# Kernel optimization log

Hardware: AMD Instinct MI355X
Metric: run time of the kernel (lower is better)

Reference implementation:

```python
import jax, jax.numpy as jnp
import numpy as np

KH = KW = 3
PAD = 1
STRIDE = 1
C_IN = 32
C_OUT = 16
H = W = 64
B = 64
H_OUT = (H - KH + 2 * PAD) // STRIDE + 1
W_OUT = (W - KW + 2 * PAD) // STRIDE + 1
S = H_OUT * W_OUT
K = C_IN * KH * KW


def unfold_2d(x):
    # x: [B, C, H, W] -> [B, C*KH*KW, S], torch.nn.functional.unfold ordering
    xp = jnp.pad(x, ((0, 0), (0, 0), (PAD, PAD), (PAD, PAD)))
    patches = []
    for i in range(KH):
        for j in range(KW):
            patches.append(xp[:, :, i:i + H_OUT * STRIDE:STRIDE, j:j + W_OUT * STRIDE:STRIDE])
    u = jnp.stack(patches, axis=2)  # [B, C, KH*KW, H_OUT, W_OUT]
    return u.reshape(x.shape[0], K, S)


def setup_inputs() -> dict:
    key = jax.random.key(0)
    k1, k2, k3 = jax.random.split(key, 3)
    X = jax.random.normal(k1, (B, C_IN, H, W), dtype=jnp.float32)
    # kaiming normal (linear): std = 1/sqrt(fan_in), fan_in = K for each location's GEMM
    weight = jax.random.normal(k2, (S, K, C_OUT), dtype=jnp.float32) / jnp.sqrt(jnp.float32(K))
    # xavier uniform over [H_OUT, W_OUT]
    lim = np.sqrt(6.0 / (H_OUT + W_OUT))
    bias = jax.random.uniform(k3, (H_OUT, W_OUT), dtype=jnp.float32, minval=-lim, maxval=lim)
    return {"X": X, "weight": weight, "bias": bias}


def reference(X, weight, bias):
    ufld = unfold_2d(X)                               # [B, K, S]
    ufld = ufld + bias.reshape(1, 1, -1)              # bias added per-location to patches
    h = jnp.einsum('bks,skc->bcs', ufld, weight)      # per-location unshared GEMM
    return h.reshape(X.shape[0], C_OUT, H_OUT, W_OUT)
```

## Files before the change

kernel.cpp:

```cpp
#include <hip/hip_runtime.h>
#include <stdint.h>
#include <stddef.h>

#define HOUT 64
#define WOUT 64
#define CIN  32
#define COUT 16
#define BATCH 64
#define SLOC 4096
#define KTOT 288
#define HPAD 66

typedef __attribute__((ext_vector_type(8))) short  short8;
typedef __attribute__((ext_vector_type(4))) float  floatx4;

static __device__ __forceinline__ unsigned short f2bf(float f) {
    union { float f; unsigned int u; } v; v.f = f;
    unsigned int u = v.u;
    unsigned int r = (u + 0x7FFFu + ((u >> 16) & 1u)) >> 16;
    return (unsigned short)r;
}

__global__ __launch_bounds__(256) void prep_kernel(const float* __restrict__ X,
                                                   unsigned short* __restrict__ xt) {
    const int id  = blockIdx.x;
    const int tid = threadIdx.x;

    if (id < 260) {
        int h1, w1;
        if (id < 66)       { h1 = 0;  w1 = id; }
        else if (id < 132) { h1 = 65; w1 = id - 66; }
        else { int r = id - 132; h1 = (r >> 1) + 1; w1 = (r & 1) ? 65 : 0; }
        ((uint4*)(xt + (size_t)(h1 * HPAD + w1) * 2048))[tid] = uint4{0u, 0u, 0u, 0u};
    }

    const int w   = tid >> 2;
    const int cg8 = (tid & 3) * 8;
#pragma unroll
    for (int u = 0; u < 2; ++u) {
        const int unit = id * 2 + u;
        const int h = unit >> 6, b = unit & 63;
        const float* xb = X + (((size_t)b * CIN + cg8) * HOUT + h) * WOUT + w;
        unsigned short v[8];
#pragma unroll
        for (int j = 0; j < 8; ++j)
            v[j] = f2bf(xb[(size_t)j * HOUT * WOUT]);
        uint4 pack;
        pack.x = (unsigned)v[0] | ((unsigned)v[1] << 16);
        pack.y = (unsigned)v[2] | ((unsigned)v[3] << 16);
        pack.z = (unsigned)v[4] | ((unsigned)v[5] << 16);
        pack.w = (unsigned)v[6] | ((unsigned)v[7] << 16);
        *(uint4*)(xt + (size_t)((h + 1) * HPAD + (w + 1)) * 2048 + b * CIN + cg8) = pack;
    }
}

__global__ __launch_bounds__(256, 4) void varconv_kernel(const unsigned short* __restrict__ xt,
                                                         const float* __restrict__ Wg,
                                                         const float* __restrict__ bias,
                                                         float* __restrict__ out) {
    __shared__ float lds[16 * 324];

    int id = blockIdx.x;
    int lo = id & 7;
    int q4 = (id >> 3) & 3;
    int g  = ((id >> 5) << 3) | lo;
    int s0 = g * 16;
    int y  = s0 >> 6;
    int x0 = s0 & 63;
    int B0 = q4 * 16;

    int lane = threadIdx.x & 63, wv = threadIdx.x >> 6;
    int q = lane >> 4;
    int n = lane & 15;

#pragma unroll
    for (int i = 0; i < 4; ++i) {
        int sl = wv * 4 + i;
        int s  = s0 + sl;
        int x  = x0 + sl;

        const unsigned short* ab = xt + (size_t)(B0 + n) * CIN + q * 8;
        short8 af[9];
#pragma unroll
        for (int t = 0; t < 9; ++t) {
            const int cy = t / 3, cx = t % 3;
            af[t] = *(const short8*)(ab + (size_t)((y + cy) * HPAD + (x + cx)) * 2048);
        }

        const float* wb = Wg + (size_t)s * (KTOT * COUT) + n;
        float csum = 0.f;
        short8 bf[9];
#pragma unroll
        for (int tg = 0; tg < 3; ++tg) {
            float wreg[3][8];
#pragma unroll
            for (int tt = 0; tt < 3; ++tt)
#pragma unroll
                for (int j = 0; j < 8; ++j)
                    wreg[tt][j] = wb[(size_t)((8 * q + j) * 9 + (tg * 3 + tt)) * COUT];
#pragma unroll
            for (int tt = 0; tt < 3; ++tt) {
                unsigned short hh[8];
#pragma unroll
                for (int j = 0; j < 8; ++j) { csum += wreg[tt][j]; hh[j] = f2bf(wreg[tt][j]); }
                union { uint4 u; short8 s8; } cv;
                cv.u.x = (unsigned)hh[0] | ((unsigned)hh[1] << 16);
                cv.u.y = (unsigned)hh[2] | ((unsigned)hh[3] << 16);
                cv.u.z = (unsigned)hh[4] | ((unsigned)hh[5] << 16);
                cv.u.w = (unsigned)hh[6] | ((unsigned)hh[7] << 16);
                bf[tg * 3 + tt] = cv.s8;
            }
        }

        csum += __shfl_xor(csum, 16, 64);
        csum += __shfl_xor(csum, 32, 64);
        float badd = bias[s] * csum;

        floatx4 acc = {0.f, 0.f, 0.f, 0.f};
#pragma unroll
        for (int t = 0; t < 9; ++t)
            acc = __builtin_amdgcn_mfma_f32_16x16x32_bf16(af[t], bf[t], acc, 0, 0, 0);

        int slot = q ^ (n & 3);
        floatx4 v = {acc[0] + badd, acc[1] + badd, acc[2] + badd, acc[3] + badd};
        *(floatx4*)&lds[n * 324 + sl * 20 + slot * 4] = v;
    }

    __syncthreads();

    int c   = lane >> 2;
    int slg = lane & 3;
#pragma unroll
    for (int i2 = 0; i2 < 4; ++i2) {
        int ib   = wv * 4 + i2;
        int slot = (ib >> 2) ^ (c & 3);
        float o0[4];
#pragma unroll
        for (int e = 0; e < 4; ++e)
            o0[e] = lds[c * 324 + (slg * 4 + e) * 20 + slot * 4 + (ib & 3)];
        floatx4 o = {o0[0], o0[1], o0[2], o0[3]};
        *(floatx4*)(out + ((size_t)((B0 + ib) * COUT + c)) * SLOC + s0 + slg * 4) = o;
    }
}

extern "C" void kernel_launch(void* const* d_in, const int* in_sizes, int n_in,
                              void* d_out, int out_size, void* d_ws, size_t ws_size,
                              hipStream_t stream) {
    const float* X    = (const float*)d_in[0];
    const float* Wg   = (const float*)d_in[1];
    const float* bias = (const float*)d_in[2];
    float* out = (float*)d_out;

    unsigned short* xt = (unsigned short*)d_ws;

    prep_kernel<<<2048, 256, 0, stream>>>(X, xt);
    varconv_kernel<<<1024, 256, 0, stream>>>(xt, Wg, bias, out);
}
```

Before: 181.7 us.

## Stage per-location weights cooperatively in LDS with double buffering

Each block now handles 8 spatial locations for all 64 batches, with one wave per 16-batch slice. Each location's weight slab is loaded once with coalesced 16-byte reads, converted to bf16 into a double-buffered LDS tile, and column sums are computed block-wide, so the next location's weights stream in while the current one computes. Before, every wave did strided scalar weight loads, and the weights were read once per batch quarter. Output is written straight from the accumulators as 8 contiguous floats per row, removing the LDS transpose. The cost is a barrier per location, fewer blocks (512), and lower occupancy from the launch bound of 2.

```diff
diff --git a/kernel.cpp b/kernel.cpp
--- a/kernel.cpp
+++ b/kernel.cpp
@@ -10,6 +10,7 @@
 #define SLOC 4096
 #define KTOT 288
 #define HPAD 66
+#define WR_STRIDE 296
 
 typedef __attribute__((ext_vector_type(8))) short  short8;
 typedef __attribute__((ext_vector_type(4))) float  floatx4;
@@ -54,93 +55,108 @@
     }
 }
 
-__global__ __launch_bounds__(256, 4) void varconv_kernel(const unsigned short* __restrict__ xt,
+__global__ __launch_bounds__(256, 2) void varconv_kernel(const unsigned short* __restrict__ xt,
                                                          const float* __restrict__ Wg,
                                                          const float* __restrict__ bias,
                                                          float* __restrict__ out) {
-    __shared__ float lds[16 * 324];
+    __shared__ unsigned short wr[2][16 * WR_STRIDE];
+    __shared__ float cs[2][4][16];
 
-    int id = blockIdx.x;
-    int lo = id & 7;
-    int q4 = (id >> 3) & 3;
-    int g  = ((id >> 5) << 3) | lo;
-    int s0 = g * 16;
-    int y  = s0 >> 6;
-    int x0 = s0 & 63;
-    int B0 = q4 * 16;
+    const int id  = blockIdx.x;
+    const int s0  = id * 8;
+    const int y   = s0 >> 6;
+    const int x0  = s0 & 63;
+    const int tid = threadIdx.x;
+    const int lane = tid & 63, wv = tid >> 6;
+    const int q = lane >> 4;
+    const int n = lane & 15;
+    const int B0 = wv * 16;
+    const int nst = (tid & 3) * 4;
 
-    int lane = threadIdx.x & 63, wv = threadIdx.x >> 6;
-    int q = lane >> 4;
-    int n = lane & 15;
+    floatx4 acc[8];
+#pragma unroll
+    for (int i = 0; i < 8; ++i) acc[i] = floatx4{0.f, 0.f, 0.f, 0.f};
+
+#define STAGE(S, BUF)                                                          \
+    {                                                                          \
+        const uint4* wsrc = (const uint4*)(Wg + (size_t)(S) * (KTOT * COUT));  \
+        float c0 = 0.f, c1 = 0.f, c2 = 0.f, c3 = 0.f;                          \
+        _Pragma("unroll")                                                      \
+        for (int it = 0; it < 5; ++it) {                                       \
+            int idx = tid + it * 256;                                          \
+            if (idx < 1152) {                                                  \
+                uint4 v = wsrc[idx];                                           \
+                int k = idx >> 2;                                              \
+                int c = (unsigned)k / 9u;                                      \
+                int t = k - c * 9;                                             \
+                unsigned short* dst = &wr[BUF][t * 32 + c];                    \
+                union { unsigned int u; float f; } a0, a1, a2, a3;             \
+                a0.u = v.x; a1.u = v.y; a2.u = v.z; a3.u = v.w;                \
+                dst[(size_t)(nst + 0) * WR_STRIDE] = f2bf(a0.f); c0 += a0.f;   \
+                dst[(size_t)(nst + 1) * WR_STRIDE] = f2bf(a1.f); c1 += a1.f;   \
+                dst[(size_t)(nst + 2) * WR_STRIDE] = f2bf(a2.f); c2 += a2.f;   \
+                dst[(size_t)(nst + 3) * WR_STRIDE] = f2bf(a3.f); c3 += a3.f;   \
+            }                                                                  \
+        }                                                                      \
+        c0 += __shfl_xor(c0, 4, 64);  c1 += __shfl_xor(c1, 4, 64);             \
+        c2 += __shfl_xor(c2, 4, 64);  c3 += __shfl_xor(c3, 4, 64);             \
+        c0 += __shfl_xor(c0, 8, 64);  c1 += __shfl_xor(c1, 8, 64);             \
+        c2 += __shfl_xor(c2, 8, 64);  c3 += __shfl_xor(c3, 8, 64);             \
+        c0 += __shfl_xor(c0, 16, 64); c1 += __shfl_xor(c1, 16, 64);            \
+        c2 += __shfl_xor(c2, 16, 64); c3 += __shfl_xor(c3, 16, 64);            \
+        c0 += __shfl_xor(c0, 32, 64); c1 += __shfl_xor(c1, 32, 64);            \
+        c2 += __shfl_xor(c2, 32, 64); c3 += __shfl_xor(c3, 32, 64);            \
+        if (lane < 4) {                                                        \
+            cs[BUF][wv][lane * 4 + 0] = c0;                                    \
+            cs[BUF][wv][lane * 4 + 1] = c1;                                    \
+            cs[BUF][wv][lane * 4 + 2] = c2;                                    \
+            cs[BUF][wv][lane * 4 + 3] = c3;                                    \
+        }                                                                      \
+    }
+
+#define COMPUTE(I, BUF)                                                        \
+    {                                                                          \
+        const int x = x0 + (I);                                                \
+        short8 af[9], bf[9];                                                   \
+        _Pragma("unroll")                                                      \
+        for (int t = 0; t < 9; ++t) {                                          \
+            const int cy = t / 3, cx = t % 3;                                  \
+            af[t] = *(const short8*)(xt +                                      \
+                (size_t)((y + cy) * HPAD + (x + cx)) * 2048 + (B0 + n) * CIN + q * 8); \
+        }                                                                      \
+        _Pragma("unroll")                                                      \
+        for (int t = 0; t < 9; ++t)                                            \
+            bf[t] = *(const short8*)&wr[BUF][n * WR_STRIDE + t * 32 + q * 8];  \
+        float badd = bias[s0 + (I)] *                                          \
+            (cs[BUF][0][n] + cs[BUF][1][n] + cs[BUF][2][n] + cs[BUF][3][n]);   \
+        _Pragma("unroll")                                                      \
+        for (int t = 0; t < 9; ++t)                                            \
+            acc[I] = __builtin_amdgcn_mfma_f32_16x16x32_bf16(af[t], bf[t], acc[I], 0, 0, 0); \
+        acc[I][0] += badd; acc[I][1] += badd;                                  \
+        acc[I][2] += badd; acc[I][3] += badd;                                  \
+    }
+
+    STAGE(s0, 0);
+    __syncthreads();
+#pragma unroll
+    for (int i = 0; i < 8; ++i) {
+        const int buf = i & 1;
+        if (i < 7) STAGE(s0 + i + 1, buf ^ 1);
+        COMPUTE(i, buf);
+        __syncthreads();
+    }
 
 #pragma unroll
-    for (int i = 0; i < 4; ++i) {
-        int sl = wv * 4 + i;
-        int s  = s0 + sl;
-        int x  = x0 + sl;
-
-        const unsigned short* ab = xt + (size_t)(B0 + n) * CIN + q * 8;
-        short8 af[9];
-#pragma unroll
-        for (int t = 0; t < 9; ++t) {
-            const int cy = t / 3, cx = t % 3;
-            af[t] = *(const short8*)(ab + (size_t)((y + cy) * HPAD + (x + cx)) * 2048);
-        }
-
-        const float* wb = Wg + (size_t)s * (KTOT * COUT) + n;
-        float csum = 0.f;
-        short8 bf[9];
-#pragma unroll
-        for (int tg = 0; tg < 3; ++tg) {
-            float wreg[3][8];
-#pragma unroll
-            for (int tt = 0; tt < 3; ++tt)
-#pragma unroll
-                for (int j = 0; j < 8; ++j)
-                    wreg[tt][j] = wb[(size_t)((8 * q + j) * 9 + (tg * 3 + tt)) * COUT];
-#pragma unroll
-            for (int tt = 0; tt < 3; ++tt) {
-                unsigned short hh[8];
-#pragma unroll
-                for (int j = 0; j < 8; ++j) { csum += wreg[tt][j]; hh[j] = f2bf(wreg[tt][j]); }
-                union { uint4 u; short8 s8; } cv;
-                cv.u.x = (unsigned)hh[0] | ((unsigned)hh[1] << 16);
-                cv.u.y = (unsigned)hh[2] | ((unsigned)hh[3] << 16);
-                cv.u.z = (unsigned)hh[4] | ((unsigned)hh[5] << 16);
-                cv.u.w = (unsigned)hh[6] | ((unsigned)hh[7] << 16);
-                bf[tg * 3 + tt] = cv.s8;
-            }
-        }
-
-        csum += __shfl_xor(csum, 16, 64);
-        csum += __shfl_xor(csum, 32, 64);
-        float badd = bias[s] * csum;
-
-        floatx4 acc = {0.f, 0.f, 0.f, 0.f};
-#pragma unroll
-        for (int t = 0; t < 9; ++t)
-            acc = __builtin_amdgcn_mfma_f32_16x16x32_bf16(af[t], bf[t], acc, 0, 0, 0);
-
-        int slot = q ^ (n & 3);
-        floatx4 v = {acc[0] + badd, acc[1] + badd, acc[2] + badd, acc[3] + badd};
-        *(floatx4*)&lds[n * 324 + sl * 20 + slot * 4] = v;
+    for (int r = 0; r < 4; ++r) {
+        const int b = B0 + 4 * q + r;
+        float* dst = out + ((size_t)(b * COUT + n)) * SLOC + s0;
+        floatx4 lo = {acc[0][r], acc[1][r], acc[2][r], acc[3][r]};
+        floatx4 hi = {acc[4][r], acc[5][r], acc[6][r], acc[7][r]};
+        *(floatx4*)dst       = lo;
+        *(floatx4*)(dst + 4) = hi;
     }
-
-    __syncthreads();
-
-    int c   = lane >> 2;
-    int slg = lane & 3;
-#pragma unroll
-    for (int i2 = 0; i2 < 4; ++i2) {
-        int ib   = wv * 4 + i2;
-        int slot = (ib >> 2) ^ (c & 3);
-        float o0[4];
-#pragma unroll
-        for (int e = 0; e < 4; ++e)
-            o0[e] = lds[c * 324 + (slg * 4 + e) * 20 + slot * 4 + (ib & 3)];
-        floatx4 o = {o0[0], o0[1], o0[2], o0[3]};
-        *(floatx4*)(out + ((size_t)((B0 + ib) * COUT + c)) * SLOC + s0 + slg * 4) = o;
-    }
+#undef STAGE
+#undef COMPUTE
 }
 
 extern "C" void kernel_launch(void* const* d_in, const int* in_sizes, int n_in,
@@ -154,5 +170,5 @@
     unsigned short* xt = (unsigned short*)d_ws;
 
     prep_kernel<<<2048, 256, 0, stream>>>(X, xt);
-    varconv_kernel<<<1024, 256, 0, stream>>>(xt, Wg, bias, out);
+    varconv_kernel<<<512, 256, 0, stream>>>(xt, Wg, bias, out);
 }
```

Result: faster. 170.2 us (-6.3%).

## Stage weights through LDS with coalesced vector loads and double buffering

Applied to the files above, without the earlier changes.

The conv kernel now has each block cover 8 locations across all 64 batches using 8 waves. Weight slabs are loaded once per location with coalesced uint4 loads, converted to bf16 pairs into a padded LDS buffer, and their column sums are reduced with shuffles. The LDS buffer is double-buffered so staging of the next location overlaps the MFMA work on the current one. Before, each of the four batch-quarter blocks re-read the same weights with strided scalar loads. The output staging through LDS is removed in favour of direct float4 stores, and the change adds more __syncthreads calls and LDS traffic per block.

```diff
diff --git a/kernel.cpp b/kernel.cpp
--- a/kernel.cpp
+++ b/kernel.cpp
@@ -6,10 +6,10 @@
 #define WOUT 64
 #define CIN  32
 #define COUT 16
-#define BATCH 64
 #define SLOC 4096
 #define KTOT 288
 #define HPAD 66
+#define WPAD 148
 
 typedef __attribute__((ext_vector_type(8))) short  short8;
 typedef __attribute__((ext_vector_type(4))) float  floatx4;
@@ -54,92 +54,106 @@
     }
 }
 
-__global__ __launch_bounds__(256, 4) void varconv_kernel(const unsigned short* __restrict__ xt,
+__global__ __launch_bounds__(512, 4) void varconv_kernel(const unsigned short* __restrict__ xt,
                                                          const float* __restrict__ Wg,
                                                          const float* __restrict__ bias,
                                                          float* __restrict__ out) {
-    __shared__ float lds[16 * 324];
+    __shared__ __align__(16) unsigned int wru[2][2][16 * WPAD];
+    __shared__ float cs[2][2][4][16];
 
-    int id = blockIdx.x;
-    int lo = id & 7;
-    int q4 = (id >> 3) & 3;
-    int g  = ((id >> 5) << 3) | lo;
-    int s0 = g * 16;
-    int y  = s0 >> 6;
-    int x0 = s0 & 63;
-    int B0 = q4 * 16;
+    const int id   = blockIdx.x;
+    const int s0   = id * 8;
+    const int y    = s0 >> 6;
+    const int x0   = s0 & 63;
+    const int tid  = threadIdx.x;
+    const int lane = tid & 63;
+    const int wv   = tid >> 6;
+    const int q4   = wv & 3;
+    const int sh   = wv >> 2;
+    const int gtid = q4 * 64 + lane;
+    const int q    = lane >> 4;
+    const int n    = lane & 15;
+    const int B0   = q4 * 16;
 
-    int lane = threadIdx.x & 63, wv = threadIdx.x >> 6;
-    int q = lane >> 4;
-    int n = lane & 15;
+    floatx4 acc[4];
+#pragma unroll
+    for (int i = 0; i < 4; ++i) acc[i] = floatx4{0.f, 0.f, 0.f, 0.f};
 
+    auto stage = [&](int P, int BUF) {
+        const int S = s0 + 4 * sh + P;
+        const uint4* wsrc = (const uint4*)(Wg + (size_t)S * (KTOT * COUT));
+        unsigned int* wb = &wru[BUF][sh][0];
+        float cacc[4] = {0.f, 0.f, 0.f, 0.f};
 #pragma unroll
-    for (int i = 0; i < 4; ++i) {
-        int sl = wv * 4 + i;
-        int s  = s0 + sl;
-        int x  = x0 + sl;
+        for (int it = 0; it < 3; ++it) {
+            const int tau = gtid + it * 256;
+            if (tau < 576) {
+                const int ng = tau & 3;
+                const int cp = (tau >> 2) & 15;
+                const int t  = tau >> 6;
+                const int kA = 18 * cp + t;
+                union { uint4 u; float f[4]; } fA, fB;
+                fA.u = wsrc[kA * 4 + ng];
+                fB.u = wsrc[(kA + 9) * 4 + ng];
+#pragma unroll
+                for (int m = 0; m < 4; ++m) {
+                    cacc[m] += fA.f[m] + fB.f[m];
+                    wb[(4 * ng + m) * WPAD + t * 16 + cp] =
+                        (unsigned)f2bf(fA.f[m]) | ((unsigned)f2bf(fB.f[m]) << 16);
+                }
+            }
+        }
+#pragma unroll
+        for (int m = 0; m < 4; ++m) {
+            cacc[m] += __shfl_xor(cacc[m], 4, 64);
+            cacc[m] += __shfl_xor(cacc[m], 8, 64);
+            cacc[m] += __shfl_xor(cacc[m], 16, 64);
+            cacc[m] += __shfl_xor(cacc[m], 32, 64);
+        }
+        if (lane < 4) {
+#pragma unroll
+            for (int m = 0; m < 4; ++m)
+                cs[BUF][sh][q4][4 * lane + m] = cacc[m];
+        }
+    };
 
-        const unsigned short* ab = xt + (size_t)(B0 + n) * CIN + q * 8;
-        short8 af[9];
+    auto compute = [&](int P, int BUF, floatx4& a) {
+        const int sl = 4 * sh + P;
+        const int S  = s0 + sl;
+        const int x  = x0 + sl;
+        short8 af[9], bf[9];
 #pragma unroll
         for (int t = 0; t < 9; ++t) {
             const int cy = t / 3, cx = t % 3;
-            af[t] = *(const short8*)(ab + (size_t)((y + cy) * HPAD + (x + cx)) * 2048);
+            af[t] = *(const short8*)(xt + (size_t)((y + cy) * HPAD + (x + cx)) * 2048
+                                        + (B0 + n) * CIN + q * 8);
         }
-
-        const float* wb = Wg + (size_t)s * (KTOT * COUT) + n;
-        float csum = 0.f;
-        short8 bf[9];
-#pragma unroll
-        for (int tg = 0; tg < 3; ++tg) {
-            float wreg[3][8];
-#pragma unroll
-            for (int tt = 0; tt < 3; ++tt)
-#pragma unroll
-                for (int j = 0; j < 8; ++j)
-                    wreg[tt][j] = wb[(size_t)((8 * q + j) * 9 + (tg * 3 + tt)) * COUT];
-#pragma unroll
-            for (int tt = 0; tt < 3; ++tt) {
-                unsigned short hh[8];
-#pragma unroll
-                for (int j = 0; j < 8; ++j) { csum += wreg[tt][j]; hh[j] = f2bf(wreg[tt][j]); }
-                union { uint4 u; short8 s8; } cv;
-                cv.u.x = (unsigned)hh[0] | ((unsigned)hh[1] << 16);
-                cv.u.y = (unsigned)hh[2] | ((unsigned)hh[3] << 16);
-                cv.u.z = (unsigned)hh[4] | ((unsigned)hh[5] << 16);
-                cv.u.w = (unsigned)hh[6] | ((unsigned)hh[7] << 16);
-                bf[tg * 3 + tt] = cv.s8;
-            }
-        }
-
-        csum += __shfl_xor(csum, 16, 64);
-        csum += __shfl_xor(csum, 32, 64);
-        float badd = bias[s] * csum;
-
-        floatx4 acc = {0.f, 0.f, 0.f, 0.f};
 #pragma unroll
         for (int t = 0; t < 9; ++t)
-            acc = __builtin_amdgcn_mfma_f32_16x16x32_bf16(af[t], bf[t], acc, 0, 0, 0);
+            bf[t] = *(const short8*)&wru[BUF][sh][n * WPAD + t * 16 + 4 * q];
+        const float badd = bias[S] * (cs[BUF][sh][0][n] + cs[BUF][sh][1][n]
+                                    + cs[BUF][sh][2][n] + cs[BUF][sh][3][n]);
+#pragma unroll
+        for (int t = 0; t < 9; ++t)
+            a = __builtin_amdgcn_mfma_f32_16x16x32_bf16(af[t], bf[t], a, 0, 0, 0);
+        a[0] += badd; a[1] += badd; a[2] += badd; a[3] += badd;
+    };
 
-        int slot = q ^ (n & 3);
-        floatx4 v = {acc[0] + badd, acc[1] + badd, acc[2] + badd, acc[3] + badd};
-        *(floatx4*)&lds[n * 324 + sl * 20 + slot * 4] = v;
+    stage(0, 0);
+    __syncthreads();
+#pragma unroll
+    for (int p = 0; p < 4; ++p) {
+        const int buf = p & 1;
+        if (p < 3) stage(p + 1, buf ^ 1);
+        compute(p, buf, acc[p]);
+        __syncthreads();
     }
 
-    __syncthreads();
-
-    int c   = lane >> 2;
-    int slg = lane & 3;
 #pragma unroll
-    for (int i2 = 0; i2 < 4; ++i2) {
-        int ib   = wv * 4 + i2;
-        int slot = (ib >> 2) ^ (c & 3);
-        float o0[4];
-#pragma unroll
-        for (int e = 0; e < 4; ++e)
-            o0[e] = lds[c * 324 + (slg * 4 + e) * 20 + slot * 4 + (ib & 3)];
-        floatx4 o = {o0[0], o0[1], o0[2], o0[3]};
-        *(floatx4*)(out + ((size_t)((B0 + ib) * COUT + c)) * SLOC + s0 + slg * 4) = o;
+    for (int r = 0; r < 4; ++r) {
+        const int b = B0 + 4 * q + r;
+        float* dst = out + ((size_t)(b * COUT + n)) * SLOC + s0 + 4 * sh;
+        *(floatx4*)dst = floatx4{acc[0][r], acc[1][r], acc[2][r], acc[3][r]};
     }
 }
 
@@ -154,5 +168,5 @@
     unsigned short* xt = (unsigned short*)d_ws;
 
     prep_kernel<<<2048, 256, 0, stream>>>(X, xt);
-    varconv_kernel<<<1024, 256, 0, stream>>>(xt, Wg, bias, out);
+    varconv_kernel<<<512, 512, 0, stream>>>(xt, Wg, bias, out);
 }
```

New measurement: 165.4 us. 1.1x faster.
